# Kernel tuning notes

Measured on AMD Instinct MI355X. Metric: run time of the kernel, lower is better.

The kernel has to match this reference:

```python
import jax, jax.numpy as jnp
import numpy as np

NUM_HEADS = 16
D_MODEL = 1024
HEAD_DIM = D_MODEL // NUM_HEADS  # 64
NEG_INF = -1e9


def alibi_bidirectional_bias(num_heads, seq_len, dtype=jnp.float32):
    """[num_heads, S, S] bias: first H/2 heads forward-causal ALiBi, last H/2 backward."""
    half = num_heads // 2
    base = 24.0 ** (1.0 / half)
    slopes = (1.0 / base ** jnp.arange(1, half + 1, dtype=dtype))[:, None, None]  # [half,1,1]
    pos = jnp.arange(seq_len)
    rel = (pos[None, :] - pos[:, None]).astype(dtype)  # rel[i,j] = j - i
    neg = jnp.full((seq_len, seq_len), NEG_INF, dtype=dtype)
    fwd = slopes * jnp.tril(rel) + jnp.triu(neg, 1)          # causal (attend past)
    bwd = slopes * jnp.triu(-rel) + jnp.tril(neg, -1)        # anti-causal (attend future)
    return jnp.concatenate([fwd, bwd], axis=0)  # [H, S, S]


def setup_inputs() -> dict:
    key = jax.random.key(0)
    ks = jax.random.split(key, 9)
    B, S, D = 2, 2048, D_MODEL
    sc = 1.0 / np.sqrt(D)
    inp = {"x": jax.random.normal(ks[0], (B, S, D), dtype=jnp.float32)}
    inp["Wq"] = jax.random.normal(ks[1], (D, D), dtype=jnp.float32) * sc
    inp["bq"] = jnp.zeros((D,), dtype=jnp.float32)
    inp["Wk"] = jax.random.normal(ks[2], (D, D), dtype=jnp.float32) * sc
    inp["bk"] = jnp.zeros((D,), dtype=jnp.float32)
    inp["Wv"] = jax.random.normal(ks[3], (D, D), dtype=jnp.float32) * sc
    inp["bv"] = jnp.zeros((D,), dtype=jnp.float32)
    inp["Wf"] = jax.random.normal(ks[4], (D, D), dtype=jnp.float32) * sc
    inp["bf"] = jnp.zeros((D,), dtype=jnp.float32)
    return inp


def reference(x, Wq, bq, Wk, bk, Wv, bv, Wf, bf):
    B, S, D = x.shape
    H, hd = NUM_HEADS, HEAD_DIM

    def heads(y):  # [B,S,D] -> [B,H,S,hd]
        return y.reshape(B, S, H, hd).transpose(0, 2, 1, 3)

    q = heads(x @ Wq + bq)
    k = heads(x @ Wk + bk)
    v = heads(x @ Wv + bv)

    bias = alibi_bidirectional_bias(H, S, x.dtype)  # [H,S,S]
    scores = jnp.einsum("bhqd,bhkd->bhqk", q, k) * (1.0 / np.sqrt(hd)) + bias[None]
    attn = jax.nn.softmax(scores, axis=-1)
    out = jnp.einsum("bhqk,bhkd->bhqd", attn, v)
    out = out.transpose(0, 2, 1, 3).reshape(B, S, D)
    return out @ Wf + bf
```

## Files before the change

### kernel.cpp

```cpp
#include <hip/hip_runtime.h>

#define S_LEN 2048
#define NH 16
#define HD 64
#define DM 1024
#define BSZ 2

typedef __bf16 bf16;
typedef __bf16 bf16x8 __attribute__((ext_vector_type(8)));
typedef float f32x4 __attribute__((ext_vector_type(4)));
typedef const unsigned int __attribute__((address_space(1)))* gas_ptr;
typedef unsigned int __attribute__((address_space(3)))* las_ptr;

__device__ __forceinline__ void gl_lds16(const bf16* g, bf16* l) {
  __builtin_amdgcn_global_load_lds((gas_ptr)g, (las_ptr)l, 16, 0, 0);
}

#define CFENCE asm volatile("" ::: "memory")

__global__ __launch_bounds__(256) void k_prep(
    const float* __restrict__ x, bf16* __restrict__ xb,
    const float* __restrict__ W0, const float* __restrict__ W1,
    const float* __restrict__ W2, const float* __restrict__ W3,
    bf16* __restrict__ dqkv, bf16* __restrict__ df) {
  __shared__ float t[64][65];
  const int id = blockIdx.x;
  if (id < 4096) {
    int i = id * 256 + threadIdx.x;
    float4 v = ((const float4*)x)[i];
    union { ushort4 u; bf16 b[4]; } o;
    o.b[0] = (bf16)v.x; o.b[1] = (bf16)v.y; o.b[2] = (bf16)v.z; o.b[3] = (bf16)v.w;
    ((ushort4*)xb)[i] = o.u;
    return;
  }
  const int id2 = id - 4096;
  const int z = id2 >> 8;
  const float* W = (z == 0) ? W0 : (z == 1) ? W1 : (z == 2) ? W2 : W3;
  bf16* D = (z < 3) ? (dqkv + (size_t)z * 1048576) : df;
  int k0 = ((id2 >> 4) & 15) * 64, n0 = (id2 & 15) * 64;
  int c = threadIdx.x & 63, rr = threadIdx.x >> 6;
#pragma unroll
  for (int it = 0; it < 16; ++it) {
    int r = it * 4 + rr;
    t[r][c] = W[(size_t)(k0 + r) * DM + n0 + c];
  }
  __syncthreads();
#pragma unroll
  for (int it = 0; it < 16; ++it) {
    int r = it * 4 + rr;
    D[(size_t)(n0 + r) * DM + k0 + c] = (bf16)t[c][r];
  }
}

template <int MODE, int BM, int BN>
__global__ __launch_bounds__(256) void k_gemm(
    const bf16* __restrict__ A, const bf16* __restrict__ Bt,
    const float* __restrict__ b0, const float* __restrict__ b1,
    const float* __restrict__ b2, void* __restrict__ Cout,
    bf16* __restrict__ VtOut, int M, int N, int K) {
  constexpr int NST = BM / 32 + BN / 32;
  __shared__ __align__(16) bf16 SA[2][BM * 64];
  __shared__ __align__(16) bf16 SB[2][BN * 64];
  constexpr int MIc = BM / 32, NIc = BN / 32;
  const int tid = threadIdx.x;
  const int l = tid & 63, w = tid >> 6;
  const int lm = l & 15, lg = l >> 4;
  const int id = blockIdx.x;
  const int xcd = id & 7, r2 = id >> 3;
  int bx, by;
  if (MODE == 0) {
    bx = (xcd & 3) * 8 + (r2 & 7);
    by = (xcd >> 2) * 12 + (r2 >> 3);
  } else {
    bx = (xcd & 3) * 16 + (r2 & 15);
    by = (xcd >> 2) * 4 + (r2 >> 4);
  }
  const int bm = bx * BM, bn = by * BN;
  const int wm = (w >> 1) * (BM / 2), wn = (w & 1) * (BN / 2);

  f32x4 acc[MIc][NIc] = {};
  const bf16* Ag = A + (size_t)bm * K;
  const bf16* Bg = Bt + (size_t)bn * K;

  auto stage = [&](int k0, int bufi) {
#pragma unroll
    for (int it = 0; it < BM / 32; ++it) {
      int cl = it * 256 + tid;
      int row = cl >> 3;
      int cs = ((cl & 7) ^ (row & 7)) << 3;
      gl_lds16(Ag + (size_t)row * K + k0 + cs, &SA[bufi][(it * 256 + w * 64) * 8]);
    }
#pragma unroll
    for (int it = 0; it < BN / 32; ++it) {
      int cl = it * 256 + tid;
      int row = cl >> 3;
      int cs = ((cl & 7) ^ (row & 7)) << 3;
      gl_lds16(Bg + (size_t)row * K + k0 + cs, &SB[bufi][(it * 256 + w * 64) * 8]);
    }
  };

  stage(0, 0);
  const int nk = K >> 6;
  int buf = 0;
  for (int t = 0; t < nk; ++t) {
    if (t + 1 < nk) {
      stage((t + 1) << 6, buf ^ 1);
      if constexpr (NST == 8) {
        asm volatile("s_waitcnt vmcnt(8)" ::: "memory");
      } else {
        asm volatile("s_waitcnt vmcnt(6)" ::: "memory");
      }
    } else {
      asm volatile("s_waitcnt vmcnt(0)" ::: "memory");
    }
    __builtin_amdgcn_s_barrier();
    CFENCE;
    const bf16* As = SA[buf];
    const bf16* Bs = SB[buf];
#pragma unroll
    for (int kk = 0; kk < 2; ++kk) {
      bf16x8 af[MIc], bfr[NIc];
#pragma unroll
      for (int mi = 0; mi < MIc; ++mi) {
        int row = wm + mi * 16 + lm;
        af[mi] = *(const bf16x8*)&As[row * 64 + ((((kk << 2) + lg) ^ (row & 7)) << 3)];
      }
#pragma unroll
      for (int ni = 0; ni < NIc; ++ni) {
        int row = wn + ni * 16 + lm;
        bfr[ni] = *(const bf16x8*)&Bs[row * 64 + ((((kk << 2) + lg) ^ (row & 7)) << 3)];
      }
#pragma unroll
      for (int mi = 0; mi < MIc; ++mi)
#pragma unroll
        for (int ni = 0; ni < NIc; ++ni)
          acc[mi][ni] = __builtin_amdgcn_mfma_f32_16x16x32_bf16(
              af[mi], bfr[ni], acc[mi][ni], 0, 0, 0);
    }
    CFENCE;
    __builtin_amdgcn_s_barrier();
    CFENCE;
    buf ^= 1;
  }

  if (MODE == 0 && bn >= 2048) {
    bf16* sc = (bf16*)SA;
#pragma unroll
    for (int ni = 0; ni < NIc; ++ni) {
      int n_l = wn + ni * 16 + lm;
      float bv = b2[(bn + n_l) & 1023];
#pragma unroll
      for (int mi = 0; mi < MIc; ++mi) {
        int g = ((wm + mi * 16) >> 2) + lg;
        int gp = g ^ ((n_l & 7) << 2);
        union { ushort4 u; bf16 bb[4]; } pkv;
#pragma unroll
        for (int r = 0; r < 4; ++r) pkv.bb[r] = (bf16)(acc[mi][ni][r] + bv);
        *(ushort4*)&sc[n_l * 128 + gp * 4] = pkv.u;
      }
    }
    __syncthreads();
    const int bq = bm >> 11, s0 = bm & 2047;
#pragma unroll
    for (int it2 = 0; it2 < 8; ++it2) {
      int row = it2 * 16 + (tid >> 4), c = tid & 15;
      int g0p = (2 * c) ^ ((row & 7) << 2);
      float4 val = *(const float4*)&sc[row * 128 + g0p * 4];
      int ng = bn + row;
      int hV = (ng >> 6) & 15;
      int d = ng & 63;
      *(float4*)&VtOut[((size_t)(bq * NH + hV) * HD + d) * S_LEN + s0 + c * 8] = val;
    }
    return;
  }

#pragma unroll
  for (int ni = 0; ni < NIc; ++ni) {
    int n = bn + wn + ni * 16 + lm;
    float bv;
    if (MODE == 0) {
      bv = (n < 1024) ? b0[n] : b1[n & 1023];
    } else {
      bv = b0[n];
    }
#pragma unroll
    for (int mi = 0; mi < MIc; ++mi) {
#pragma unroll
      for (int r = 0; r < 4; ++r) {
        int m = bm + wm + mi * 16 + lg * 4 + r;
        float v = acc[mi][ni][r] + bv;
        if (MODE == 0) {
          int qkv = n >> 10;
          int h = (n >> 6) & 15;
          int d = n & 63;
          int b = m >> 11, s = m & 2047;
          ((bf16*)Cout)[(size_t)qkv * (BSZ * NH * S_LEN * HD) +
                        ((size_t)(b * NH + h) * S_LEN + s) * HD + d] = (bf16)v;
        } else {
          ((float*)Cout)[(size_t)m * N + n] = v;
        }
      }
    }
  }
}

#define SMX(MASKED)                                                           \
  {                                                                           \
    const float t0 = slp2 * (float)dlo;                                       \
    _Pragma("unroll") for (int ni = 0; ni < 4; ++ni) {                        \
      const int koff = (ni & 1) * 32 + (ni >> 1) * 4;                         \
      float bni = t0 + dni[ni];                                               \
      float pr[4];                                                            \
      _Pragma("unroll") for (int r = 0; r < 4; ++r) {                         \
        float v = fmaf(sc[ni][r], c1, bni + srr[r]);                          \
        if (MASKED) {                                                         \
          int reli = dlo + koff + relc + r;                                   \
          bool ok = causal ? (reli <= 0) : (reli >= 0);                       \
          v = ok ? v : -1e9f;                                                 \
        }                                                                     \
        pr[r] = __builtin_amdgcn_exp2f(v);                                    \
      }                                                                       \
      union { bf16 b[2]; unsigned u; } u0, u1;                                \
      u0.b[0] = (bf16)pr[0]; u0.b[1] = (bf16)pr[1];                           \
      u1.b[0] = (bf16)pr[2]; u1.b[1] = (bf16)pr[3];                           \
      pk[ni][0] = u0.u; pk[ni][1] = u1.u;                                     \
    }                                                                         \
  }

__global__ __launch_bounds__(512, 2) void k_attn(const bf16* __restrict__ Qh,
                                                 const bf16* __restrict__ Kh,
                                                 const bf16* __restrict__ Vt,
                                                 bf16* __restrict__ O) {
  __shared__ __align__(16) bf16 Ks[2][4096];
  __shared__ __align__(16) bf16 Vs[2][4096];
  const int id = blockIdx.x;
  const int bh = ((id & 7) << 2) | ((id >> 3) & 3);
  const int pid = id >> 5;
  const int b = bh >> 4, h = bh & 15;
  const bool causal = (h < 8);
  const int tid = threadIdx.x;
  const int w = tid >> 6, l = tid & 63;
  const int lm = l & 15, lg = l >> 4;
  const int hh = causal ? h : h - 8;
  const float c1 = 0.18033688f;
  const float sm = __builtin_amdgcn_exp2f(-(float)(hh + 1) * 0.57312035f) * 1.44269504f;
  const float slp2 = causal ? sm : -sm;
  const int relc = lg * 8 - lm;
  const int krow_lane = ((lm >> 2) << 3) + (lm & 3);
  const int swzK = (lm & 3) | (((lm >> 2) & 1) << 2);
  const int swzV = (lm & 3) | (((lm >> 3) & 1) << 2);
  float dni[4], srr[4];
#pragma unroll
  for (int ni = 0; ni < 4; ++ni)
    dni[ni] = slp2 * (float)((ni & 1) * 32 + (ni >> 1) * 4);
#pragma unroll
  for (int r = 0; r < 4; ++r) srr[r] = slp2 * (float)(relc + r);

  const bf16* Qp = Qh + (size_t)bh * S_LEN * HD;
  const bf16* Kp = Kh + (size_t)bh * S_LEN * HD;
  const bf16* Vp = Vt + (size_t)bh * HD * S_LEN;

  bf16x8 ones;
#pragma unroll
  for (int i = 0; i < 8; ++i) ones[i] = (bf16)1.0f;

  auto stage = [&](bf16* lk, bf16* lv, int j0) {
    const int row = tid >> 3, c = tid & 7;
    const int sw = (row & 3) | (((row >> 3) & 1) << 2);
    const int gc = (c ^ sw) << 3;
    const int clb8 = ((tid >> 6) << 6) * 8;
    gl_lds16(Kp + (size_t)(j0 + row) * HD + gc, lk + clb8);
    gl_lds16(Vp + (size_t)row * S_LEN + j0 + gc, lv + clb8);
  };

  auto run_strip = [&](int yi) {
    const int qb = yi << 7;
    const int q0 = qb + w * 16;
    const int jbase = causal ? 0 : qb;
    const int jcnt = causal ? (qb >> 6) + 2 : ((S_LEN - qb) >> 6);

    bf16x8 qf[2];
#pragma unroll
    for (int kk = 0; kk < 2; ++kk)
      qf[kk] = *(const bf16x8*)&Qp[(size_t)(q0 + lm) * HD + kk * 32 + lg * 8];

    f32x4 oacc[4] = {};
    f32x4 lacc = {};

    auto compute = [&](int t, const bf16* lk, const bf16* lv) {
      const int j0 = jbase + t * 64;
      const int dlo = j0 - q0;
      const bool skip = causal ? (dlo >= 16) : (dlo <= -64);
      if (skip) return;
      f32x4 sc[4] = {};
#pragma unroll
      for (int kk = 0; kk < 2; ++kk)
#pragma unroll
        for (int ni = 0; ni < 4; ++ni) {
          const int koff = (ni & 1) * 32 + (ni >> 1) * 4;
          bf16x8 kf = *(const bf16x8*)&lk[(koff + krow_lane) * 64 +
                                          ((((kk << 2) + lg) ^ swzK) << 3)];
          sc[ni] = __builtin_amdgcn_mfma_f32_16x16x32_bf16(kf, qf[kk], sc[ni],
                                                           0, 0, 0);
        }
      bf16x8 vf[2][4];
#pragma unroll
      for (int kk = 0; kk < 2; ++kk)
#pragma unroll
        for (int di = 0; di < 4; ++di)
          vf[kk][di] = *(const bf16x8*)&lv[(di * 16 + lm) * 64 +
                                           ((((kk << 2) + lg) ^ swzV) << 3)];
      const bool full = causal ? (dlo <= -63) : (dlo >= 15);
      unsigned pk[4][2];
      if (full) { SMX(false); } else { SMX(true); }
#pragma unroll
      for (int kk = 0; kk < 2; ++kk) {
        union { unsigned d[4]; bf16x8 v; } pa;
        pa.d[0] = pk[kk][0];
        pa.d[1] = pk[kk][1];
        pa.d[2] = pk[kk + 2][0];
        pa.d[3] = pk[kk + 2][1];
        lacc = __builtin_amdgcn_mfma_f32_16x16x32_bf16(pa.v, ones, lacc, 0, 0, 0);
#pragma unroll
        for (int di = 0; di < 4; ++di)
          oacc[di] = __builtin_amdgcn_mfma_f32_16x16x32_bf16(pa.v, vf[kk][di],
                                                             oacc[di], 0, 0, 0);
      }
    };

    stage(Ks[0], Vs[0], jbase);
    asm volatile("s_waitcnt vmcnt(0)" ::: "memory");
    __builtin_amdgcn_s_barrier();
    CFENCE;

    for (int t = 0; t < jcnt - 1; ++t) {
      const int cur = t & 1;
      stage(Ks[cur ^ 1], Vs[cur ^ 1], jbase + (t + 1) * 64);
      asm volatile("s_waitcnt vmcnt(2)" ::: "memory");
      __builtin_amdgcn_s_barrier();
      CFENCE;
      compute(t, Ks[cur], Vs[cur]);
      CFENCE;
      __builtin_amdgcn_s_barrier();
      CFENCE;
    }
    asm volatile("s_waitcnt vmcnt(0)" ::: "memory");
    __builtin_amdgcn_s_barrier();
    CFENCE;
    compute(jcnt - 1, Ks[(jcnt - 1) & 1], Vs[(jcnt - 1) & 1]);
    CFENCE;
    __builtin_amdgcn_s_barrier();
    CFENCE;

    float rin[4];
#pragma unroll
    for (int r = 0; r < 4; ++r) rin[r] = 1.0f / lacc[r];
#pragma unroll
    for (int di = 0; di < 4; ++di) {
      int d = h * HD + di * 16 + lm;
#pragma unroll
      for (int r = 0; r < 4; ++r) {
        int q = q0 + lg * 4 + r;
        O[((size_t)b * S_LEN + q) * DM + d] = (bf16)(oacc[di][r] * rin[r]);
      }
    }
  };

  run_strip(pid);
  run_strip(15 - pid);
}

extern "C" void kernel_launch(void* const* d_in, const int* in_sizes, int n_in,
                              void* d_out, int out_size, void* d_ws, size_t ws_size,
                              hipStream_t stream) {
  const float* x  = (const float*)d_in[0];
  const float* Wq = (const float*)d_in[1];
  const float* bq = (const float*)d_in[2];
  const float* Wk = (const float*)d_in[3];
  const float* bk = (const float*)d_in[4];
  const float* Wv = (const float*)d_in[5];
  const float* bv = (const float*)d_in[6];
  const float* Wf = (const float*)d_in[7];
  const float* bfp = (const float*)d_in[8];

  char* ws = (char*)d_ws;
  const size_t MB = 1ull << 20;
  bf16* xb    = (bf16*)(ws);
  bf16* Wqkvt = (bf16*)(ws + 8 * MB);
  bf16* Wft   = (bf16*)(ws + 14 * MB);
  bf16* QKVh  = (bf16*)(ws + 16 * MB);
  bf16* Vt    = (bf16*)(ws + 40 * MB);
  bf16* O     = QKVh + 2 * 4194304;

  k_prep<<<5120, 256, 0, stream>>>(x, xb, Wq, Wk, Wv, Wf, Wqkvt, Wft);
  k_gemm<0, 128, 128><<<768, 256, 0, stream>>>(
      xb, Wqkvt, bq, bk, bv, QKVh, Vt, 4096, 3072, 1024);
  k_attn<<<256, 512, 0, stream>>>(QKVh, QKVh + 4194304, Vt, O);
  k_gemm<2, 64, 128><<<512, 256, 0, stream>>>(
      O, Wft, bfp, bfp, bfp, d_out, nullptr, 4096, 1024, 1024);
}
```

Before: 182.8 us.

## Split attention strips into separate blocks with longest-first scheduling order

Each attention block now handles one 128-query strip instead of a paired strip, doubling the grid to 512 blocks. Blocks are ordered so the heaviest strips (long causal/anti-causal ranges) are dispatched first for better load balance. The pipeline loop is also simplified to use __syncthreads with a conditional prefetch, replacing the explicit vmcnt waits. This trades the per-block balance of pairing with more blocks and dynamic scheduling, and it relies on __syncthreads waiting for outstanding LDS loads.

New measurement: 183.2 us. No clear change (+0.2%).

```diff
diff --git a/kernel.cpp b/kernel.cpp
--- a/kernel.cpp
+++ b/kernel.cpp
@@ -234,10 +234,12 @@
   __shared__ __align__(16) bf16 Ks[2][4096];
   __shared__ __align__(16) bf16 Vs[2][4096];
   const int id = blockIdx.x;
-  const int bh = ((id & 7) << 2) | ((id >> 3) & 3);
-  const int pid = id >> 5;
+  const int lam = id >> 3;
+  const int bh = ((id & 7) << 2) | (lam & 3);
+  const int rho = (lam < 32) ? (lam >> 2) : 15 - ((lam - 32) >> 2);
   const int b = bh >> 4, h = bh & 15;
   const bool causal = (h < 8);
+  const int yi = causal ? (15 - rho) : rho;
   const int tid = threadIdx.x;
   const int w = tid >> 6, l = tid & 63;
   const int lm = l & 15, lg = l >> 4;
@@ -273,101 +275,81 @@
     gl_lds16(Vp + (size_t)row * S_LEN + j0 + gc, lv + clb8);
   };
 
-  auto run_strip = [&](int yi) {
-    const int qb = yi << 7;
-    const int q0 = qb + w * 16;
-    const int jbase = causal ? 0 : qb;
-    const int jcnt = causal ? (qb >> 6) + 2 : ((S_LEN - qb) >> 6);
-
-    bf16x8 qf[2];
+  const int qb = yi << 7;
+  const int q0 = qb + w * 16;
+  const int jbase = causal ? 0 : qb;
+  const int jcnt = causal ? (qb >> 6) + 2 : ((S_LEN - qb) >> 6);
+
+  bf16x8 qf[2];
+#pragma unroll
+  for (int kk = 0; kk < 2; ++kk)
+    qf[kk] = *(const bf16x8*)&Qp[(size_t)(q0 + lm) * HD + kk * 32 + lg * 8];
+
+  f32x4 oacc[4] = {};
+  f32x4 lacc = {};
+
+  auto compute = [&](int t, const bf16* lk, const bf16* lv) {
+    const int j0 = jbase + t * 64;
+    const int dlo = j0 - q0;
+    const bool skip = causal ? (dlo >= 16) : (dlo <= -64);
+    if (skip) return;
+    f32x4 sc[4] = {};
 #pragma unroll
     for (int kk = 0; kk < 2; ++kk)
-      qf[kk] = *(const bf16x8*)&Qp[(size_t)(q0 + lm) * HD + kk * 32 + lg * 8];
-
-    f32x4 oacc[4] = {};
-    f32x4 lacc = {};
-
-    auto compute = [&](int t, const bf16* lk, const bf16* lv) {
-      const int j0 = jbase + t * 64;
-      const int dlo = j0 - q0;
-      const bool skip = causal ? (dlo >= 16) : (dlo <= -64);
-      if (skip) return;
-      f32x4 sc[4] = {};
-#pragma unroll
-      for (int kk = 0; kk < 2; ++kk)
-#pragma unroll
-        for (int ni = 0; ni < 4; ++ni) {
-          const int koff = (ni & 1) * 32 + (ni >> 1) * 4;
-          bf16x8 kf = *(const bf16x8*)&lk[(koff + krow_lane) * 64 +
-                                          ((((kk << 2) + lg) ^ swzK) << 3)];
-          sc[ni] = __builtin_amdgcn_mfma_f32_16x16x32_bf16(kf, qf[kk], sc[ni],
-                                                           0, 0, 0);
-        }
-      bf16x8 vf[2][4];
-#pragma unroll
-      for (int kk = 0; kk < 2; ++kk)
-#pragma unroll
-        for (int di = 0; di < 4; ++di)
-          vf[kk][di] = *(const bf16x8*)&lv[(di * 16 + lm) * 64 +
-                                           ((((kk << 2) + lg) ^ swzV) << 3)];
-      const bool full = causal ? (dlo <= -63) : (dlo >= 15);
-      unsigned pk[4][2];
-      if (full) { SMX(false); } else { SMX(true); }
-#pragma unroll
-      for (int kk = 0; kk < 2; ++kk) {
-        union { unsigned d[4]; bf16x8 v; } pa;
-        pa.d[0] = pk[kk][0];
-        pa.d[1] = pk[kk][1];
-        pa.d[2] = pk[kk + 2][0];
-        pa.d[3] = pk[kk + 2][1];
-        lacc = __builtin_amdgcn_mfma_f32_16x16x32_bf16(pa.v, ones, lacc, 0, 0, 0);
-#pragma unroll
-        for (int di = 0; di < 4; ++di)
-          oacc[di] = __builtin_amdgcn_mfma_f32_16x16x32_bf16(pa.v, vf[kk][di],
-                                                             oacc[di], 0, 0, 0);
-      }
-    };
-
-    stage(Ks[0], Vs[0], jbase);
-    asm volatile("s_waitcnt vmcnt(0)" ::: "memory");
-    __builtin_amdgcn_s_barrier();
-    CFENCE;
-
-    for (int t = 0; t < jcnt - 1; ++t) {
-      const int cur = t & 1;
-      stage(Ks[cur ^ 1], Vs[cur ^ 1], jbase + (t + 1) * 64);
-      asm volatile("s_waitcnt vmcnt(2)" ::: "memory");
-      __builtin_amdgcn_s_barrier();
-      CFENCE;
-      compute(t, Ks[cur], Vs[cur]);
-      CFENCE;
-      __builtin_amdgcn_s_barrier();
-      CFENCE;
-    }
-    asm volatile("s_waitcnt vmcnt(0)" ::: "memory");
-    __builtin_amdgcn_s_barrier();
-    CFENCE;
-    compute(jcnt - 1, Ks[(jcnt - 1) & 1], Vs[(jcnt - 1) & 1]);
-    CFENCE;
-    __builtin_amdgcn_s_barrier();
-    CFENCE;
-
-    float rin[4];
-#pragma unroll
-    for (int r = 0; r < 4; ++r) rin[r] = 1.0f / lacc[r];
-#pragma unroll
-    for (int di = 0; di < 4; ++di) {
-      int d = h * HD + di * 16 + lm;
-#pragma unroll
-      for (int r = 0; r < 4; ++r) {
-        int q = q0 + lg * 4 + r;
-        O[((size_t)b * S_LEN + q) * DM + d] = (bf16)(oacc[di][r] * rin[r]);
-      }
+#pragma unroll
+      for (int ni = 0; ni < 4; ++ni) {
+        const int koff = (ni & 1) * 32 + (ni >> 1) * 4;
+        bf16x8 kf = *(const bf16x8*)&lk[(koff + krow_lane) * 64 +
+                                        ((((kk << 2) + lg) ^ swzK) << 3)];
+        sc[ni] = __builtin_amdgcn_mfma_f32_16x16x32_bf16(kf, qf[kk], sc[ni],
+                                                         0, 0, 0);
+      }
+    bf16x8 vf[2][4];
+#pragma unroll
+    for (int kk = 0; kk < 2; ++kk)
+#pragma unroll
+      for (int di = 0; di < 4; ++di)
+        vf[kk][di] = *(const bf16x8*)&lv[(di * 16 + lm) * 64 +
+                                         ((((kk << 2) + lg) ^ swzV) << 3)];
+    const bool full = causal ? (dlo <= -63) : (dlo >= 15);
+    unsigned pk[4][2];
+    if (full) { SMX(false); } else { SMX(true); }
+#pragma unroll
+    for (int kk = 0; kk < 2; ++kk) {
+      union { unsigned d[4]; bf16x8 v; } pa;
+      pa.d[0] = pk[kk][0];
+      pa.d[1] = pk[kk][1];
+      pa.d[2] = pk[kk + 2][0];
+      pa.d[3] = pk[kk + 2][1];
+      lacc = __builtin_amdgcn_mfma_f32_16x16x32_bf16(pa.v, ones, lacc, 0, 0, 0);
+#pragma unroll
+      for (int di = 0; di < 4; ++di)
+        oacc[di] = __builtin_amdgcn_mfma_f32_16x16x32_bf16(pa.v, vf[kk][di],
+                                                           oacc[di], 0, 0, 0);
     }
   };
 
-  run_strip(pid);
-  run_strip(15 - pid);
+  stage(Ks[0], Vs[0], jbase);
+  __syncthreads();
+  for (int t = 0; t < jcnt; ++t) {
+    const int cur = t & 1;
+    if (t + 1 < jcnt) stage(Ks[cur ^ 1], Vs[cur ^ 1], jbase + (t + 1) * 64);
+    compute(t, Ks[cur], Vs[cur]);
+    __syncthreads();
+  }
+
+  float rin[4];
+#pragma unroll
+  for (int r = 0; r < 4; ++r) rin[r] = 1.0f / lacc[r];
+#pragma unroll
+  for (int di = 0; di < 4; ++di) {
+    int d = h * HD + di * 16 + lm;
+#pragma unroll
+    for (int r = 0; r < 4; ++r) {
+      int q = q0 + lg * 4 + r;
+      O[((size_t)b * S_LEN + q) * DM + d] = (bf16)(oacc[di][r] * rin[r]);
+    }
+  }
 }
 
 extern "C" void kernel_launch(void* const* d_in, const int* in_sizes, int n_in,
@@ -395,7 +377,7 @@
   k_prep<<<5120, 256, 0, stream>>>(x, xb, Wq, Wk, Wv, Wf, Wqkvt, Wft);
   k_gemm<0, 128, 128><<<768, 256, 0, stream>>>(
       xb, Wqkvt, bq, bk, bv, QKVh, Vt, 4096, 3072, 1024);
-  k_attn<<<256, 512, 0, stream>>>(QKVh, QKVh + 4194304, Vt, O);
+  k_attn<<<512, 512, 0, stream>>>(QKVh, QKVh + 4194304, Vt, O);
   k_gemm<2, 64, 128><<<512, 256, 0, stream>>>(
       O, Wft, bfp, bfp, bfp, d_out, nullptr, 4096, 1024, 1024);
 }
```
